# Optimization experiments

Hardware: AMD Instinct MI355X
Metric: run time of the kernel (lower is better)

The kernel has to match this reference:

```python
import jax, jax.numpy as jnp
import numpy as np

N, D, E = 200000, 256, 6400000
RATIO = 0.5
NEG_SLOPE = 0.2


def _xavier(key, shape, gain=1.414):
    fan_in, fan_out = shape[0], shape[1]
    limit = gain * (6.0 / (fan_in + fan_out)) ** 0.5
    return jax.random.uniform(key, shape, jnp.float32, -limit, limit)


def setup_inputs() -> dict:
    key = jax.random.key(0)
    ks = jax.random.split(key, 8)
    x = jax.random.normal(ks[0], (N, D), jnp.float32)
    edge_index = jax.random.randint(ks[1], (2, E), 0, N, dtype=jnp.int64)
    return {
        "x": x,
        "edge_index": edge_index,
        "w_s1": _xavier(ks[2], (2 * D, D)), "b_s1": jnp.zeros((D,), jnp.float32),
        "w_s2": _xavier(ks[3], (D, 1)),     "b_s2": jnp.zeros((1,), jnp.float32),
        "w_f1": _xavier(ks[4], (D, D // 2)), "b_f1": jnp.zeros((D // 2,), jnp.float32),
        "w_f2": _xavier(ks[5], (D // 2, 1)), "b_f2": jnp.zeros((1,), jnp.float32),
        "w_p": _xavier(ks[6], (D, D)),      "b_p": jnp.zeros((D,), jnp.float32),
        "alpha": jnp.float32(0.5), "beta": jnp.float32(0.5),
    }


def reference(x, edge_index, w_s1, b_s1, w_s2, b_s2, w_f1, b_f1, w_f2, b_f2, w_p, b_p, alpha, beta):
    num_nodes = x.shape[0]
    k = max(1, int(RATIO * num_nodes))
    lrelu = lambda v: jax.nn.leaky_relu(v, NEG_SLOPE)

    row, col = edge_index[0], edge_index[1]
    # degree(row, N): scatter-add of ones over source nodes
    deg = jax.ops.segment_sum(jnp.ones_like(row, dtype=x.dtype), row, num_segments=num_nodes)
    # F.normalize(p=2, dim=0) on the [N,1] degree column
    deg_norm = deg / jnp.maximum(jnp.sqrt(jnp.sum(deg * deg)), 1e-12)

    struct_in = jnp.concatenate([x, jnp.broadcast_to(deg_norm[:, None], x.shape)], axis=1)  # [N, 2D]
    struct_scores = (lrelu(struct_in @ w_s1 + b_s1) @ w_s2 + b_s2)[:, 0]  # dropout is eval no-op
    feat_scores = (lrelu(x @ w_f1 + b_f1) @ w_f2 + b_f2)[:, 0]

    a = jax.nn.sigmoid(alpha)
    b = jax.nn.sigmoid(beta)
    s = a + b
    scores = (a / s) * struct_scores + (b / s) * feat_scores  # [N]

    # single-graph top-k (batch=None default path)
    topk_scores, topk_idx = jax.lax.top_k(scores, k)
    x_pooled = lrelu(x[topk_idx] @ w_p + b_p)  # post_pool, dropout no-op

    # edge remap + compaction (valid edges first, -1 padding to keep static shape)
    node_map = jnp.full((num_nodes,), -1, dtype=jnp.int32).at[topk_idx].set(
        jnp.arange(k, dtype=jnp.int32))
    mr, mc = node_map[row], node_map[col]
    mask = (mr >= 0) & (mc >= 0)
    order = jnp.argsort(~mask, stable=True)  # stable: keeps original edge order among valid
    edge_index_pooled = jnp.stack([
        jnp.where(mask, mr, -1)[order],
        jnp.where(mask, mc, -1)[order],
    ])
    return x_pooled, edge_index_pooled, topk_scores
```

## Files before the change

### kernel.cpp

```cpp
#include <hip/hip_runtime.h>
#include <math.h>

typedef unsigned long long u64;
typedef unsigned int u32;
typedef unsigned short u16;
typedef __attribute__((ext_vector_type(8))) short bf16x8;
typedef __attribute__((ext_vector_type(4))) float f32x4;

#define D   256
#define ECH 16
#define EBLK (256*ECH)
#define BAND_W 2048
#define BAND_DELTA 1e-3f
#define HR  50176
#define HCH 64
#define NBUCK 65536

__device__ __forceinline__ double lrelu(double v){ return v > 0.0 ? v : 0.2*v; }
__device__ __forceinline__ float  lreluf(float v){ return v > 0.0f ? v : 0.2f*v; }

__device__ __forceinline__ u16 f2bf(float f){
  union{float f; u32 u;} v; v.f = f;
  u32 r = v.u + 0x7FFFu + ((v.u >> 16) & 1u);
  return (u16)(r >> 16);
}
__device__ __forceinline__ float bf2f(u16 b){
  union{u32 u; float f;} v; v.u = ((u32)b) << 16; return v.f;
}

__global__ __launch_bounds__(256) void k_deghist(const int* __restrict__ row, int E,
                                                 u32* __restrict__ partial, int NR){
  __shared__ u32 h[HR/4];
  const int tid = threadIdx.x;
  const int r = blockIdx.x % NR;
  const int c = blockIdx.x / NR;
  for (int i = tid; i < HR/4; i += 256) h[i] = 0;
  __syncthreads();
  const int lo = r * HR;
  int CE = ((E + HCH - 1) / HCH + 3) & ~3;
  const int e0 = c * CE;
  const int e1 = min(e0 + CE, E);
  for (int e = e0 + tid*4; e < e1; e += 256*4){
    if (e + 3 < e1){
      int4 v = *(const int4*)(row + e);
      u32 d0 = (u32)(v.x - lo), d1 = (u32)(v.y - lo);
      u32 d2 = (u32)(v.z - lo), d3 = (u32)(v.w - lo);
      if (d0 < (u32)HR) atomicAdd(&h[d0 >> 2], 1u << ((d0 & 3)*8));
      if (d1 < (u32)HR) atomicAdd(&h[d1 >> 2], 1u << ((d1 & 3)*8));
      if (d2 < (u32)HR) atomicAdd(&h[d2 >> 2], 1u << ((d2 & 3)*8));
      if (d3 < (u32)HR) atomicAdd(&h[d3 >> 2], 1u << ((d3 & 3)*8));
    } else {
      for (int j = 0; j < 4 && e + j < e1; ++j){
        u32 d = (u32)(row[e+j] - lo);
        if (d < (u32)HR) atomicAdd(&h[d >> 2], 1u << ((d & 3)*8));
      }
    }
  }
  __syncthreads();
  u32* plane = partial + (size_t)blockIdx.x * (HR/4);
  for (int i = tid; i < HR/4; i += 256) plane[i] = h[i];
}

__global__ void k_degred2(const u32* __restrict__ partial, int N, int NR,
                          int* __restrict__ deg, u64* __restrict__ out){
  __shared__ u64 sh[256];
  u64 local = 0;
  int stride = gridDim.x*blockDim.x;
  for (int i = blockIdx.x*blockDim.x + threadIdx.x; i < N; i += stride){
    int r = i / HR, off = i % HR;
    const int word = off >> 2, shift = (off & 3)*8;
    u32 s = 0;
    #pragma unroll 8
    for (int c = 0; c < HCH; ++c)
      s += (partial[(size_t)(c*NR + r)*(HR/4) + word] >> shift) & 0xFFu;
    deg[i] = (int)s;
    local += (u64)s * (u64)s;
  }
  sh[threadIdx.x] = local; __syncthreads();
  for (int s = 128; s > 0; s >>= 1){
    if (threadIdx.x < s) sh[threadIdx.x] += sh[threadIdx.x+s];
    __syncthreads();
  }
  if (threadIdx.x == 0) atomicAdd(out, sh[0]);
}

__global__ void k_prep_wsw(const float* __restrict__ wS1, const float* __restrict__ wF1,
                           const float* __restrict__ wP,
                           const float* __restrict__ alpha, const float* __restrict__ beta,
                           const u64* __restrict__ sumsq,
                           u16* __restrict__ wswH, u16* __restrict__ wswL,
                           u16* __restrict__ wPH,
                           double* __restrict__ s1b, double* __restrict__ scal,
                           float* __restrict__ s1bf, float* __restrict__ scalf){
  const int b = blockIdx.x;
  if (b < 384){
    int idx = b*256 + threadIdx.x;
    int i    = idx & 7;
    int lane = (idx >> 3) & 63;
    int sg   = (idx >> 9) & 7;
    int t    = idx >> 12;
    int k = sg*32 + ((lane >> 4) & 3)*8 + i;
    int c16 = lane & 15;
    float wv;
    if (t < 16) wv = wS1[k*256 + t*16 + c16];
    else        wv = wF1[k*128 + (t-16)*16 + c16];
    u16 h = f2bf(wv);
    wswH[idx] = h;
    wswL[idx] = f2bf(wv - bf2f(h));
  } else if (b < 640){
    int idx = (b-384)*256 + threadIdx.x;
    int i    = idx & 7;
    int lane = (idx >> 3) & 63;
    int sg   = (idx >> 9) & 7;
    int t    = idx >> 12;
    int k = sg*32 + ((lane >> 4) & 3)*8 + i;
    wPH[idx] = f2bf(wP[k*256 + t*16 + (lane & 15)]);
  } else {
    int j = threadIdx.x;
    double s = 0.0;
    for (int r = 0; r < D; ++r) s += (double)wS1[(D + r)*D + j];
    s1b[j] = s;
    s1bf[j] = (float)s;
    if (j == 0){
      double a = 1.0/(1.0 + exp(-(double)alpha[0]));
      double bb = 1.0/(1.0 + exp(-(double)beta[0]));
      scal[0] = a/(a+bb);
      scal[1] = bb/(a+bb);
      double dn = sqrt((double)(*sumsq));
      scal[2] = dn > 1e-12 ? dn : 1e-12;
      scalf[0] = (float)scal[0];
      scalf[1] = (float)scal[1];
      scalf[2] = (float)(1.0/scal[2]);
    }
  }
}

__global__ __launch_bounds__(512, 4) void k_scores_mfma(
    const float* __restrict__ x, const int* __restrict__ deg,
    const u16* __restrict__ wswH, const u16* __restrict__ wswL,
    const float* __restrict__ bS1, const float* __restrict__ wS2, const float* __restrict__ bS2,
    const float* __restrict__ bF1, const float* __restrict__ wF2, const float* __restrict__ bF2,
    const float* __restrict__ s1bf, const float* __restrict__ scalf,
    float* __restrict__ s32, u64* __restrict__ keysrc, u32* __restrict__ kmm, int N)
{
  __shared__ u16 xsh[2][4096];
  __shared__ u16 xsl[2][4096];
  __shared__ float dnsh[64];
  __shared__ float part_s[64][9];
  __shared__ float part_f[64][9];

  const int tid  = threadIdx.x;
  const int lane = tid & 63;
  const int w    = tid >> 6;
  const int node0 = blockIdx.x * 64;

  if (tid < 64){
    int node = node0 + tid;
    dnsh[tid] = (node < N) ? ((float)deg[node] * scalf[2]) : 0.0f;
  }

  const int row_st = tid >> 3;
  const int seg_st = tid & 7;
  const int unit_w = row_st*8 + (seg_st ^ (row_st & 7));
  const float* srcbase = x + (size_t)(node0 + row_st)*D + seg_st*8;
  const bool rv = (node0 + row_st) < N;

  f32x4 acc[4][3];
  #pragma unroll
  for (int m = 0; m < 4; ++m)
    #pragma unroll
    for (int n = 0; n < 3; ++n) acc[m][n] = (f32x4){0.f,0.f,0.f,0.f};

  float xr[8];
  {
    if (rv){
      float4 a = *(const float4*)(srcbase);
      float4 b = *(const float4*)(srcbase + 4);
      xr[0]=a.x; xr[1]=a.y; xr[2]=a.z; xr[3]=a.w;
      xr[4]=b.x; xr[5]=b.y; xr[6]=b.z; xr[7]=b.w;
    } else {
      #pragma unroll
      for (int i = 0; i < 8; ++i) xr[i] = 0.f;
    }
  }

  #pragma unroll
  for (int c = 0; c < 4; ++c){
    const int pb = c & 1;
    {
      u16 h[8];
      #pragma unroll
      for (int i = 0; i < 8; ++i) h[i] = f2bf(xr[i]);
      uint4 H; H.x = (u32)h[0] | ((u32)h[1]<<16); H.y = (u32)h[2] | ((u32)h[3]<<16);
               H.z = (u32)h[4] | ((u32)h[5]<<16); H.w = (u32)h[6] | ((u32)h[7]<<16);
      u16 l[8];
      #pragma unroll
      for (int i = 0; i < 8; ++i) l[i] = f2bf(xr[i] - bf2f(h[i]));
      uint4 L; L.x = (u32)l[0] | ((u32)l[1]<<16); L.y = (u32)l[2] | ((u32)l[3]<<16);
               L.z = (u32)l[4] | ((u32)l[5]<<16); L.w = (u32)l[6] | ((u32)l[7]<<16);
      *(uint4*)&xsh[pb][unit_w*8] = H;
      *(uint4*)&xsl[pb][unit_w*8] = L;
    }
    __syncthreads();
    if (c < 3){
      const float* sn = srcbase + (c+1)*64;
      if (rv){
        float4 a = *(const float4*)(sn);
        float4 b = *(const float4*)(sn + 4);
        xr[0]=a.x; xr[1]=a.y; xr[2]=a.z; xr[3]=a.w;
        xr[4]=b.x; xr[5]=b.y; xr[6]=b.z; xr[7]=b.w;
      }
    }
    #pragma unroll
    for (int s = 0; s < 2; ++s){
      const int sg = c*2 + s;
      bf16x8 ah[4], al[4];
      #pragma unroll
      for (int mt = 0; mt < 4; ++mt){
        int row = mt*16 + (lane & 15);
        int seg = s*4 + (lane >> 4);
        int un  = row*8 + (seg ^ (row & 7));
        ah[mt] = *(const bf16x8*)&xsh[pb][un*8];
        al[mt] = *(const bf16x8*)&xsl[pb][un*8];
      }
      const int t0 = w*3;
      size_t o0 = ((size_t)(t0*8 + sg)*64 + lane)*8;
      bf16x8 bh = *(const bf16x8*)&wswH[o0];
      bf16x8 bl = *(const bf16x8*)&wswL[o0];
      #pragma unroll
      for (int nt = 0; nt < 3; ++nt){
        bf16x8 nbh = bh, nbl = bl;
        if (nt < 2){
          size_t on = ((size_t)((t0+nt+1)*8 + sg)*64 + lane)*8;
          nbh = *(const bf16x8*)&wswH[on];
          nbl = *(const bf16x8*)&wswL[on];
        }
        #pragma unroll
        for (int mt = 0; mt < 4; ++mt){
          acc[mt][nt] = __builtin_amdgcn_mfma_f32_16x16x32_bf16(ah[mt], bh, acc[mt][nt], 0,0,0);
          acc[mt][nt] = __builtin_amdgcn_mfma_f32_16x16x32_bf16(al[mt], bh, acc[mt][nt], 0,0,0);
          acc[mt][nt] = __builtin_amdgcn_mfma_f32_16x16x32_bf16(ah[mt], bl, acc[mt][nt], 0,0,0);
        }
        bh = nbh; bl = nbl;
      }
    }
    if (c < 3) __syncthreads();
  }

  float dnl[4][4];
  #pragma unroll
  for (int mt = 0; mt < 4; ++mt)
    #pragma unroll
    for (int j = 0; j < 4; ++j)
      dnl[mt][j] = dnsh[mt*16 + (lane>>4)*4 + j];

  float ps[4][4], pf[4][4];
  #pragma unroll
  for (int mt = 0; mt < 4; ++mt)
    #pragma unroll
    for (int j = 0; j < 4; ++j){ ps[mt][j] = 0.f; pf[mt][j] = 0.f; }

  #pragma unroll
  for (int nt = 0; nt < 3; ++nt){
    const int t = w*3 + nt;
    const int c16 = lane & 15;
    const bool isS = (t < 16);
    const int col = isS ? t*16 + c16 : (t-16)*16 + c16;
    const float bias = isS ? bS1[col] : bF1[col];
    const float sbv  = isS ? s1bf[col] : 0.f;
    const float vv   = isS ? wS2[col] : wF2[col];
    #pragma unroll
    for (int mt = 0; mt < 4; ++mt){
      #pragma unroll
      for (int j = 0; j < 4; ++j){
        float v = acc[mt][nt][j] + bias + dnl[mt][j]*sbv;
        v = lreluf(v) * vv;
        v += __shfl_xor(v, 1);
        v += __shfl_xor(v, 2);
        v += __shfl_xor(v, 4);
        v += __shfl_xor(v, 8);
        if (isS) ps[mt][j] += v; else pf[mt][j] += v;
      }
    }
  }
  if ((lane & 15) == 0){
    #pragma unroll
    for (int mt = 0; mt < 4; ++mt)
      #pragma unroll
      for (int j = 0; j < 4; ++j){
        int row = mt*16 + (lane>>4)*4 + j;
        part_s[row][w] = ps[mt][j];
        part_f[row][w] = pf[mt][j];
      }
  }
  __syncthreads();
  if (tid < 64){
    int node = node0 + tid;
    u32 key32mn = 0xFFFFFFFFu, key32mx = 0u;
    if (node < N){
      float sv = 0.f, fv = 0.f;
      #pragma unroll
      for (int ww = 0; ww < 8; ++ww){ sv += part_s[tid][ww]; fv += part_f[tid][ww]; }
      float sc = scalf[0]*(sv + bS2[0]) + scalf[1]*(fv + bF2[0]);
      s32[node] = sc;
      u32 bits = __float_as_uint(sc);
      u32 ord = (bits >> 31) ? ~bits : (bits | 0x80000000u);
      u32 key32 = ~ord;
      keysrc[node] = ((u64)key32 << 32) | (u32)node;
      key32mn = key32; key32mx = key32;
    }
    #pragma unroll
    for (int off = 32; off > 0; off >>= 1){
      u32 on = __shfl_xor(key32mn, off);
      u32 ox = __shfl_xor(key32mx, off);
      key32mn = min(key32mn, on);
      key32mx = max(key32mx, ox);
    }
    if (tid == 0){
      atomicMin(&kmm[0], key32mn);
      atomicMax(&kmm[1], key32mx);
    }
  }
}

__global__ void k_hist(const u64* __restrict__ keysrc, int N,
                       const u32* __restrict__ kmm, u32* __restrict__ hist){
  const u32 kmin = kmm[0];
  const u64 rng = (u64)(kmm[1] - kmm[0]) + 1;
  int stride = gridDim.x*blockDim.x;
  for (int i = blockIdx.x*blockDim.x + threadIdx.x; i < N; i += stride){
    u32 key = (u32)(keysrc[i] >> 32);
    u32 b = (u32)((((u64)(key - kmin)) << 16) / rng);
    atomicAdd(&hist[b], 1u);
  }
}

__global__ __launch_bounds__(1024) void k_scan64k(const u32* __restrict__ hist,
                                                  u32* __restrict__ boff){
  __shared__ u32 ts[1024];
  const int t = threadIdx.x;
  u32 loc[64];
  u32 s = 0;
  const uint4* hp = (const uint4*)(hist + t*64);
  #pragma unroll
  for (int i = 0; i < 16; ++i){
    uint4 v = hp[i];
    loc[i*4+0]=v.x; loc[i*4+1]=v.y; loc[i*4+2]=v.z; loc[i*4+3]=v.w;
    s += v.x + v.y + v.z + v.w;
  }
  ts[t] = s; __syncthreads();
  for (int d = 1; d < 1024; d <<= 1){
    u32 v = (t >= d) ? ts[t-d] : 0;
    __syncthreads();
    ts[t] += v;
    __syncthreads();
  }
  u32 run = ts[t] - s;
  u32* bp = boff + t*64;
  #pragma unroll 8
  for (int i = 0; i < 64; ++i){ bp[i] = run; run += loc[i]; }
}

__global__ void k_scatter(const u64* __restrict__ keysrc, int N,
                          const u32* __restrict__ kmm, u32* __restrict__ boff,
                          u64* __restrict__ keyS){
  const u32 kmin = kmm[0];
  const u64 rng = (u64)(kmm[1] - kmm[0]) + 1;
  int stride = gridDim.x*blockDim.x;
  for (int i = blockIdx.x*blockDim.x + threadIdx.x; i < N; i += stride){
    u64 kv = keysrc[i];
    u32 key = (u32)(kv >> 32);
    u32 b = (u32)((((u64)(key - kmin)) << 16) / rng);
    u32 pos = atomicAdd(&boff[b], 1u);
    keyS[pos] = kv;
  }
}

__global__ __launch_bounds__(256) void kr_rescore(
    const u64* __restrict__ keys, const float* __restrict__ s32,
    const float* __restrict__ x, const int* __restrict__ deg,
    const float* __restrict__ wS1, const float* __restrict__ bS1,
    const float* __restrict__ wS2, const float* __restrict__ bS2,
    const float* __restrict__ wF1, const float* __restrict__ bF1,
    const float* __restrict__ wF2, const float* __restrict__ bF2,
    const double* __restrict__ s1b, const double* __restrict__ scal,
    u32* __restrict__ r01, double* __restrict__ bandS, int k, int N)
{
  const int r = k - BAND_W + blockIdx.x;
  if (r < 0 || r >= N) return;
  u32 kk32 = (u32)(keys[k-1] >> 32);
  u32 kord = ~kk32;
  u32 ku = (kord & 0x80000000u) ? (kord ^ 0x80000000u) : ~kord;
  const float ccut = __uint_as_float(ku);
  const int node = (int)(u32)(keys[r] & 0xFFFFFFFFULL);
  const float s = s32[node];
  if (s < ccut - BAND_DELTA || s > ccut + BAND_DELTA){
    if (threadIdx.x == 0) bandS[blockIdx.x] = (double)s;
    return;
  }

  const int tid = threadIdx.x;
  if (tid == 0){ atomicMin(&r01[0], (u32)r); atomicMax(&r01[1], (u32)r); }

  __shared__ float xr[256];
  __shared__ double rsp[4], rfp[4];
  xr[tid] = x[(size_t)node*D + tid];
  __syncthreads();

  const int j = tid;
  double a0=0.0, a1=0.0, a2=0.0, a3=0.0;
  double b0=0.0, b1=0.0, b2=0.0, b3=0.0;
  if (j < 128){
    for (int rr = 0; rr < D; rr += 4){
      double x0 = (double)xr[rr+0], x1 = (double)xr[rr+1];
      double x2 = (double)xr[rr+2], x3 = (double)xr[rr+3];
      a0 = fma(x0, (double)wS1[(rr+0)*D + j], a0);
      a1 = fma(x1, (double)wS1[(rr+1)*D + j], a1);
      a2 = fma(x2, (double)wS1[(rr+2)*D + j], a2);
      a3 = fma(x3, (double)wS1[(rr+3)*D + j], a3);
      b0 = fma(x0, (double)wF1[(rr+0)*128 + j], b0);
      b1 = fma(x1, (double)wF1[(rr+1)*128 + j], b1);
      b2 = fma(x2, (double)wF1[(rr+2)*128 + j], b2);
      b3 = fma(x3, (double)wF1[(rr+3)*128 + j], b3);
    }
  } else {
    for (int rr = 0; rr < D; rr += 4){
      double x0 = (double)xr[rr+0], x1 = (double)xr[rr+1];
      double x2 = (double)xr[rr+2], x3 = (double)xr[rr+3];
      a0 = fma(x0, (double)wS1[(rr+0)*D + j], a0);
      a1 = fma(x1, (double)wS1[(rr+1)*D + j], a1);
      a2 = fma(x2, (double)wS1[(rr+2)*D + j], a2);
      a3 = fma(x3, (double)wS1[(rr+3)*D + j], a3);
    }
  }
  double accA = ((a0+a1)+(a2+a3)) + (double)bS1[j] + ((double)deg[node]/scal[2]) * s1b[j];
  double sp = lrelu(accA) * (double)wS2[j];
  double fp = 0.0;
  if (j < 128){
    double accB = ((b0+b1)+(b2+b3)) + (double)bF1[j];
    fp = lrelu(accB) * (double)wF2[j];
  }

  const int lane = tid & 63, wave = tid >> 6;
  #pragma unroll
  for (int off = 32; off > 0; off >>= 1){
    sp += __shfl_down(sp, off);
    fp += __shfl_down(fp, off);
  }
  if (lane == 0){ rsp[wave] = sp; rfp[wave] = fp; }
  __syncthreads();
  if (tid == 0){
    double SP = rsp[0]+rsp[1]+rsp[2]+rsp[3];
    double FP = rfp[0]+rfp[1]+rfp[2]+rfp[3];
    bandS[blockIdx.x] = scal[0]*(SP + (double)bS2[0]) + scal[1]*(FP + (double)bF2[0]);
  }
}

__global__ __launch_bounds__(1024) void kr_bandsort(u64* __restrict__ keys,
    const double* __restrict__ bandS, const u32* __restrict__ r01, int k){
  __shared__ double bs[4096];
  __shared__ int bi[4096];
  if (r01[0] == 0xFFFFFFFFu) return;
  const int r0 = (int)r01[0], r1 = (int)r01[1];
  int nb = r1 - r0 + 1;
  if (nb <= 1) return;
  if (nb > 4096) nb = 4096;
  int M = 1; while (M < nb) M <<= 1;
  const int tid = threadIdx.x;
  const int sbase = r0 - (k - BAND_W);
  for (int m = tid; m < M; m += 1024){
    if (m < nb){ bs[m] = bandS[sbase + m]; bi[m] = (int)(u32)(keys[r0+m] & 0xFFFFFFFFULL); }
    else       { bs[m] = -1.0/0.0;         bi[m] = 0x7FFFFFFF; }
  }
  __syncthreads();
  for (int size = 2; size <= M; size <<= 1){
    for (int stride = size >> 1; stride > 0; stride >>= 1){
      for (int p = tid; p < (M >> 1); p += 1024){
        int i = 2*p - (p & (stride-1));
        int jj = i + stride;
        bool up = ((i & size) == 0);
        double si_ = bs[i], sj = bs[jj];
        int ii = bi[i], ij = bi[jj];
        bool gt = (si_ < sj) || (si_ == sj && ii > ij);
        if (gt == up){ bs[i]=sj; bs[jj]=si_; bi[i]=ij; bi[jj]=ii; }
      }
      __syncthreads();
    }
  }
  for (int m = tid; m < nb; m += 1024)
    keys[r0+m] = (u64)(u32)bi[m];
}

__global__ void k_finalize(const u64* __restrict__ keys, const float* __restrict__ s32,
                           int k, int* __restrict__ nmap, float* __restrict__ outS){
  int p = blockIdx.x*blockDim.x + threadIdx.x;
  if (p < k){
    int node = (int)(u32)(keys[p] & 0xFFFFFFFFULL);
    nmap[node] = p;
    outS[p] = s32[node];
  }
}

__global__ __launch_bounds__(512, 4) void k_xpool_mfma(
    const float* __restrict__ x, const u64* __restrict__ keys,
    const u16* __restrict__ wH,
    const float* __restrict__ bP, float* __restrict__ out, int kk)
{
  __shared__ u16 xsh[2][4096];

  const int tid  = threadIdx.x;
  const int lane = tid & 63;
  const int w    = tid >> 6;
  const int p0 = blockIdx.x * 64;
  if (p0 >= kk) return;

  const int row_st = tid >> 3;
  const int seg_st = tid & 7;
  const int unit_w = row_st*8 + (seg_st ^ (row_st & 7));
  int prow = p0 + row_st; if (prow >= kk) prow = kk - 1;
  const int node = (int)(u32)(keys[prow] & 0xFFFFFFFFULL);
  const float* srcbase = x + (size_t)node*D + seg_st*8;

  f32x4 acc[4][2];
  #pragma unroll
  for (int m = 0; m < 4; ++m){ acc[m][0] = (f32x4){0.f,0.f,0.f,0.f}; acc[m][1] = (f32x4){0.f,0.f,0.f,0.f}; }

  float xr[8];
  {
    float4 a = *(const float4*)(srcbase);
    float4 b = *(const float4*)(srcbase + 4);
    xr[0]=a.x; xr[1]=a.y; xr[2]=a.z; xr[3]=a.w;
    xr[4]=b.x; xr[5]=b.y; xr[6]=b.z; xr[7]=b.w;
  }

  #pragma unroll
  for (int c = 0; c < 4; ++c){
    const int pb = c & 1;
    {
      u16 h[8];
      #pragma unroll
      for (int i = 0; i < 8; ++i) h[i] = f2bf(xr[i]);
      uint4 H; H.x = (u32)h[0] | ((u32)h[1]<<16); H.y = (u32)h[2] | ((u32)h[3]<<16);
               H.z = (u32)h[4] | ((u32)h[5]<<16); H.w = (u32)h[6] | ((u32)h[7]<<16);
      *(uint4*)&xsh[pb][unit_w*8] = H;
    }
    __syncthreads();
    if (c < 3){
      const float* sn = srcbase + (c+1)*64;
      float4 a = *(const float4*)(sn);
      float4 b = *(const float4*)(sn + 4);
      xr[0]=a.x; xr[1]=a.y; xr[2]=a.z; xr[3]=a.w;
      xr[4]=b.x; xr[5]=b.y; xr[6]=b.z; xr[7]=b.w;
    }
    #pragma unroll
    for (int s = 0; s < 2; ++s){
      const int sg = c*2 + s;
      bf16x8 ah[4];
      #pragma unroll
      for (int mt = 0; mt < 4; ++mt){
        int row = mt*16 + (lane & 15);
        int seg = s*4 + (lane >> 4);
        int un  = row*8 + (seg ^ (row & 7));
        ah[mt] = *(const bf16x8*)&xsh[pb][un*8];
      }
      const int t0 = w*2;
      size_t o0 = ((size_t)(t0*8 + sg)*64 + lane)*8;
      bf16x8 bh = *(const bf16x8*)&wH[o0];
      #pragma unroll
      for (int nt = 0; nt < 2; ++nt){
        bf16x8 nbh = bh;
        if (nt < 1){
          size_t on = ((size_t)((t0+1)*8 + sg)*64 + lane)*8;
          nbh = *(const bf16x8*)&wH[on];
        }
        #pragma unroll
        for (int mt = 0; mt < 4; ++mt)
          acc[mt][nt] = __builtin_amdgcn_mfma_f32_16x16x32_bf16(ah[mt], bh, acc[mt][nt], 0,0,0);
        bh = nbh;
      }
    }
    if (c < 3) __syncthreads();
  }

  const int c16 = lane & 15, r4 = (lane >> 4)*4;
  #pragma unroll
  for (int nt = 0; nt < 2; ++nt){
    const int col = (w*2 + nt)*16 + c16;
    const float bias = bP[col];
    #pragma unroll
    for (int mt = 0; mt < 4; ++mt){
      #pragma unroll
      for (int j = 0; j < 4; ++j){
        int p = p0 + mt*16 + r4 + j;
        if (p < kk) out[(size_t)p*D + col] = lreluf(acc[mt][nt][j] + bias);
      }
    }
  }
}

__global__ __launch_bounds__(256) void k_ecount(const int* __restrict__ erow, const int* __restrict__ ecol,
    const int* __restrict__ nmap, int E, int* __restrict__ bcount){
  __shared__ int sc[256];
  const int tid = threadIdx.x;
  const int base = blockIdx.x*EBLK + tid*ECH;
  int cnt = 0;
  #pragma unroll
  for (int q = 0; q < ECH; ++q){
    int e = base + q;
    if (e < E){
      if (nmap[erow[e]] >= 0 && nmap[ecol[e]] >= 0) cnt++;
    }
  }
  sc[tid] = cnt; __syncthreads();
  for (int s = 128; s > 0; s >>= 1){
    if (tid < s) sc[tid] += sc[tid+s];
    __syncthreads();
  }
  if (tid == 0) bcount[blockIdx.x] = sc[0];
}

__global__ __launch_bounds__(1024) void k_escan(const int* __restrict__ bcount, int nblk,
                                                int* __restrict__ boff, int* __restrict__ tot){
  __shared__ int sh[1024];
  const int tid = threadIdx.x;
  int carry = 0;
  for (int s = 0; s < nblk; s += 1024){
    int v = (s + tid < nblk) ? bcount[s+tid] : 0;
    sh[tid] = v; __syncthreads();
    for (int d = 1; d < 1024; d <<= 1){
      int t = (tid >= d) ? sh[tid-d] : 0;
      __syncthreads();
      sh[tid] += t;
      __syncthreads();
    }
    if (s + tid < nblk) boff[s+tid] = carry + sh[tid] - v;
    carry += sh[1023];
    __syncthreads();
  }
  if (tid == 0) *tot = carry;
}

__global__ void k_efill_tail(float* __restrict__ outR, float* __restrict__ outC,
                             const int* __restrict__ tot, int E){
  const int t0 = *tot;
  int stride = gridDim.x*blockDim.x;
  for (int i = t0 + blockIdx.x*blockDim.x + threadIdx.x; i < E; i += stride){
    outR[i] = -1.0f;
    outC[i] = -1.0f;
  }
}

__global__ __launch_bounds__(256) void k_escatter(const int* __restrict__ erow, const int* __restrict__ ecol,
    const int* __restrict__ nmap, int E, const int* __restrict__ boff,
    float* __restrict__ outR, float* __restrict__ outC){
  __shared__ int sc[256];
  const int tid = threadIdx.x;
  const int base = blockIdx.x*EBLK + tid*ECH;
  int mr[ECH], mc[ECH];
  int cnt = 0;
  #pragma unroll
  for (int q = 0; q < ECH; ++q){
    int e = base + q;
    int a = -1, b = -1;
    if (e < E){ a = nmap[erow[e]]; b = nmap[ecol[e]]; }
    mr[q] = a; mc[q] = b;
    if (a >= 0 && b >= 0) cnt++;
  }
  sc[tid] = cnt; __syncthreads();
  int v = cnt;
  for (int d = 1; d < 256; d <<= 1){
    int t = (tid >= d) ? sc[tid-d] : 0;
    __syncthreads();
    sc[tid] += t;
    __syncthreads();
  }
  int pos = boff[blockIdx.x] + sc[tid] - v;
  #pragma unroll
  for (int q = 0; q < ECH; ++q){
    if (mr[q] >= 0 && mc[q] >= 0){
      outR[pos] = (float)mr[q];
      outC[pos] = (float)mc[q];
      pos++;
    }
  }
}

extern "C" void kernel_launch(void* const* d_in, const int* in_sizes, int n_in,
                              void* d_out, int out_size, void* d_ws, size_t ws_size,
                              hipStream_t stream)
{
  const float* x   = (const float*)d_in[0];
  const int*   ei  = (const int*)d_in[1];
  const float* wS1 = (const float*)d_in[2];
  const float* bS1 = (const float*)d_in[3];
  const float* wS2 = (const float*)d_in[4];
  const float* bS2 = (const float*)d_in[5];
  const float* wF1 = (const float*)d_in[6];
  const float* bF1 = (const float*)d_in[7];
  const float* wF2 = (const float*)d_in[8];
  const float* bF2 = (const float*)d_in[9];
  const float* wP  = (const float*)d_in[10];
  const float* bP  = (const float*)d_in[11];
  const float* alpha = (const float*)d_in[12];
  const float* beta  = (const float*)d_in[13];
  (void)n_in; (void)out_size; (void)ws_size;

  const int N = in_sizes[0] / D;
  const int E = in_sizes[1] / 2;
  int k = (int)(0.5 * (double)N); if (k < 1) k = 1;
  const int nblk_e = (E + EBLK - 1) / EBLK;
  const int NR = (N + HR - 1) / HR;

  char* w = (char*)d_ws;
  size_t off = 0;
  auto alloc = [&](size_t bytes)->char*{
    char* p = w + off;
    off = (off + bytes + 255) & ~(size_t)255;
    return p;
  };
  float*  s32    = (float*) alloc((size_t)N*4);
  u64*    keysrc = (u64*)   alloc((size_t)N*8);
  u64*    keyS   = (u64*)   alloc((size_t)N*8);
  int*    deg    = (int*)   alloc((size_t)N*4);
  int*    nmap   = (int*)   alloc((size_t)N*4);
  u32*    kmm    = (u32*)   alloc(2*4);
  u32*    hist   = (u32*)   alloc((size_t)NBUCK*4);
  u32*    boffH  = (u32*)   alloc((size_t)NBUCK*4);
  double* s1b    = (double*)alloc((size_t)D*8);
  float*  s1bf   = (float*) alloc((size_t)D*4);
  double* scal   = (double*)alloc(4*8);
  float*  scalf  = (float*) alloc(4*4);
  u64*    sumsq  = (u64*)   alloc(8);
  u32*    r01    = (u32*)   alloc(2*4);
  int*    tot    = (int*)   alloc(4);
  double* bandS  = (double*)alloc((size_t)2*BAND_W*8);
  u16*    wswH   = (u16*)   alloc((size_t)98304*2);
  u16*    wswL   = (u16*)   alloc((size_t)98304*2);
  u16*    wswPH  = (u16*)   alloc((size_t)65536*2);
  int*    bcount = (int*)   alloc((size_t)nblk_e*4);
  int*    boff   = (int*)   alloc((size_t)nblk_e*4);

  float* outX  = (float*)d_out;
  float* outER = outX  + (size_t)k*D;
  float* outEC = outER + (size_t)E;
  float* outS  = outEC + (size_t)E;

  u32* partial = (u32*)outER;

  hipMemsetAsync(sumsq,  0,    8,               stream);
  hipMemsetAsync(nmap,   0xFF, (size_t)N*4,     stream);
  hipMemsetAsync(kmm,    0xFF, 4,               stream);
  hipMemsetAsync(kmm+1,  0x00, 4,               stream);
  hipMemsetAsync(hist,   0,    (size_t)NBUCK*4, stream);
  hipMemsetAsync(r01,    0xFF, 4,               stream);
  hipMemsetAsync(r01+1,  0x00, 4,               stream);

  k_deghist<<<NR*HCH, 256, 0, stream>>>(ei, E, partial, NR);
  k_degred2<<<1024, 256, 0, stream>>>(partial, N, NR, deg, sumsq);
  k_prep_wsw<<<641, 256, 0, stream>>>(wS1, wF1, wP, alpha, beta, sumsq,
                                      wswH, wswL, wswPH,
                                      s1b, scal, s1bf, scalf);
  k_scores_mfma<<<(N + 63)/64, 512, 0, stream>>>(x, deg, wswH, wswL,
                                                 bS1, wS2, bS2, bF1, wF2, bF2,
                                                 s1bf, scalf, s32, keysrc, kmm, N);

  k_hist   <<<(N+255)/256, 256, 0, stream>>>(keysrc, N, kmm, hist);
  k_scan64k<<<1, 1024, 0, stream>>>(hist, boffH);
  k_scatter<<<(N+255)/256, 256, 0, stream>>>(keysrc, N, kmm, boffH, keyS);

  kr_rescore <<<2*BAND_W, 256, 0, stream>>>(keyS, s32, x, deg, wS1,bS1,wS2,bS2,
                                            wF1,bF1,wF2,bF2, s1b, scal,
                                            r01, bandS, k, N);
  kr_bandsort<<<1, 1024, 0, stream>>>(keyS, bandS, r01, k);

  k_finalize<<<(k+255)/256, 256, 0, stream>>>(keyS, s32, k, nmap, outS);
  k_xpool_mfma<<<(k+63)/64, 512, 0, stream>>>(x, keyS, wswPH, bP, outX, k);
  k_ecount  <<<nblk_e, 256, 0, stream>>>(ei, ei+E, nmap, E, bcount);
  k_escan   <<<1, 1024, 0, stream>>>(bcount, nblk_e, boff, tot);
  k_efill_tail<<<1024, 256, 0, stream>>>(outER, outEC, tot, E);
  k_escatter<<<nblk_e, 256, 0, stream>>>(ei, ei+E, nmap, E, boff, outER, outEC);
}
```

Baseline: 694.1 us.

## Fuse finalize into xpool, defer score shuffles, widen degree histogram chunks

```diff
diff --git a/kernel.cpp b/kernel.cpp
--- a/kernel.cpp
+++ b/kernel.cpp
@@ -12,8 +12,8 @@
 #define EBLK (256*ECH)
 #define BAND_W 2048
 #define BAND_DELTA 1e-3f
-#define HR  50176
-#define HCH 64
+#define HR  100352
+#define HCH 128
 #define NBUCK 65536
 
 __device__ __forceinline__ double lrelu(double v){ return v > 0.0 ? v : 0.2*v; }
@@ -247,6 +247,7 @@
     if (c < 3) __syncthreads();
   }
 
+  const int c16 = lane & 15;
   float dnl[4][4];
   #pragma unroll
   for (int mt = 0; mt < 4; ++mt)
@@ -254,16 +255,15 @@
     for (int j = 0; j < 4; ++j)
       dnl[mt][j] = dnsh[mt*16 + (lane>>4)*4 + j];
 
-  float ps[4][4], pf[4][4];
+  float psv[4][4], pfv[4][4];
   #pragma unroll
   for (int mt = 0; mt < 4; ++mt)
     #pragma unroll
-    for (int j = 0; j < 4; ++j){ ps[mt][j] = 0.f; pf[mt][j] = 0.f; }
+    for (int j = 0; j < 4; ++j){ psv[mt][j] = 0.f; pfv[mt][j] = 0.f; }
 
   #pragma unroll
   for (int nt = 0; nt < 3; ++nt){
     const int t = w*3 + nt;
-    const int c16 = lane & 15;
     const bool isS = (t < 16);
     const int col = isS ? t*16 + c16 : (t-16)*16 + c16;
     const float bias = isS ? bS1[col] : bF1[col];
@@ -275,23 +275,25 @@
       for (int j = 0; j < 4; ++j){
         float v = acc[mt][nt][j] + bias + dnl[mt][j]*sbv;
         v = lreluf(v) * vv;
-        v += __shfl_xor(v, 1);
-        v += __shfl_xor(v, 2);
-        v += __shfl_xor(v, 4);
-        v += __shfl_xor(v, 8);
-        if (isS) ps[mt][j] += v; else pf[mt][j] += v;
-      }
-    }
-  }
-  if ((lane & 15) == 0){
-    #pragma unroll
-    for (int mt = 0; mt < 4; ++mt)
-      #pragma unroll
-      for (int j = 0; j < 4; ++j){
+        if (isS) psv[mt][j] += v; else pfv[mt][j] += v;
+      }
+    }
+  }
+  #pragma unroll
+  for (int mt = 0; mt < 4; ++mt){
+    #pragma unroll
+    for (int j = 0; j < 4; ++j){
+      float a = psv[mt][j], b = pfv[mt][j];
+      a += __shfl_xor(a, 1); b += __shfl_xor(b, 1);
+      a += __shfl_xor(a, 2); b += __shfl_xor(b, 2);
+      a += __shfl_xor(a, 4); b += __shfl_xor(b, 4);
+      a += __shfl_xor(a, 8); b += __shfl_xor(b, 8);
+      if (c16 == 0){
         int row = mt*16 + (lane>>4)*4 + j;
-        part_s[row][w] = ps[mt][j];
-        part_f[row][w] = pf[mt][j];
-      }
+        part_s[row][w] = a;
+        part_f[row][w] = b;
+      }
+    }
   }
   __syncthreads();
   if (tid < 64){
@@ -491,20 +493,11 @@
     keys[r0+m] = (u64)(u32)bi[m];
 }
 
-__global__ void k_finalize(const u64* __restrict__ keys, const float* __restrict__ s32,
-                           int k, int* __restrict__ nmap, float* __restrict__ outS){
-  int p = blockIdx.x*blockDim.x + threadIdx.x;
-  if (p < k){
-    int node = (int)(u32)(keys[p] & 0xFFFFFFFFULL);
-    nmap[node] = p;
-    outS[p] = s32[node];
-  }
-}
-
 __global__ __launch_bounds__(512, 4) void k_xpool_mfma(
     const float* __restrict__ x, const u64* __restrict__ keys,
-    const u16* __restrict__ wH,
-    const float* __restrict__ bP, float* __restrict__ out, int kk)
+    const u16* __restrict__ wH, const float* __restrict__ bP,
+    const float* __restrict__ s32, int* __restrict__ nmap, float* __restrict__ outS,
+    float* __restrict__ out, int kk)
 {
   __shared__ u16 xsh[2][4096];
 
@@ -513,6 +506,15 @@
   const int w    = tid >> 6;
   const int p0 = blockIdx.x * 64;
   if (p0 >= kk) return;
+
+  if (tid < 64){
+    int p = p0 + tid;
+    if (p < kk){
+      int nd = (int)(u32)(keys[p] & 0xFFFFFFFFULL);
+      nmap[nd] = p;
+      outS[p] = s32[nd];
+    }
+  }
 
   const int row_st = tid >> 3;
   const int seg_st = tid & 7;
@@ -773,8 +775,8 @@
                                             r01, bandS, k, N);
   kr_bandsort<<<1, 1024, 0, stream>>>(keyS, bandS, r01, k);
 
-  k_finalize<<<(k+255)/256, 256, 0, stream>>>(keyS, s32, k, nmap, outS);
-  k_xpool_mfma<<<(k+63)/64, 512, 0, stream>>>(x, keyS, wswPH, bP, outX, k);
+  k_xpool_mfma<<<(k+63)/64, 512, 0, stream>>>(x, keyS, wswPH, bP,
+                                              s32, nmap, outS, outX, k);
   k_ecount  <<<nblk_e, 256, 0, stream>>>(ei, ei+E, nmap, E, bcount);
   k_escan   <<<1, 1024, 0, stream>>>(bcount, nblk_e, boff, tot);
   k_efill_tail<<<1024, 256, 0, stream>>>(outER, outEC, tot, E);
```

Result: faster. 679.8 us, median of 2 (-2.1%).
